# Optimization experiments

Measured on AMD Instinct MI355X. Metric: run time of the kernel, lower is better.

Reference implementation:

```python
import jax, jax.numpy as jnp
import numpy as np

B, L, E = 4, 2048, 1024
H, D = 16, 64  # heads, head_dim; H*D == E


def setup_inputs() -> dict:
    key = jax.random.key(0)
    ks = jax.random.split(key, 6)
    s = 0.02
    return {
        "x": jax.random.normal(ks[0], (B, L, E), dtype=jnp.float32),
        "Wq": jax.random.normal(ks[1], (E, H * D), dtype=jnp.float32) * s,
        "Wk": jax.random.normal(ks[2], (E, H * D), dtype=jnp.float32) * s,
        "Wv": jax.random.normal(ks[3], (E, H * D), dtype=jnp.float32) * s,
        "Wo": jax.random.normal(ks[4], (H * D, E), dtype=jnp.float32) * s,
        "bo": jax.random.normal(ks[5], (E,), dtype=jnp.float32) * s,
    }


def reference(x, Wq, Wk, Wv, Wo, bo):
    b, l, e = x.shape
    q = (x @ Wq).reshape(b, l, H, D)
    k = (x @ Wk).reshape(b, l, H, D)
    v = (x @ Wv).reshape(b, l, H, D)
    # NOTE: original scales by sqrt(embed_size), not sqrt(head_dim)
    energy = jnp.einsum('nqhd,nkhd->nhqk', q, k)
    attn = jax.nn.softmax(energy / jnp.sqrt(jnp.float32(e)), axis=3)
    out = jnp.einsum('nhql,nlhd->nqhd', attn, v).reshape(b, l, H * D)
    return out @ Wo + bo
```

## Files before the change

### kernel.cpp

```cpp
#include <hip/hip_runtime.h>

#define B_ 4
#define L_ 2048
#define E_ 1024
#define H_ 16
#define D_ 64
#define CSCALE 0.045084960222629414f

typedef short s16x8 __attribute__((ext_vector_type(8)));
typedef short s16x4 __attribute__((ext_vector_type(4)));
typedef float f32x4 __attribute__((ext_vector_type(4)));

__device__ __forceinline__ unsigned short f2bf(float f) {
  union { float f; unsigned int u; } v;
  v.f = f;
  unsigned int u = v.u;
  u += 0x7fffu + ((u >> 16) & 1u);
  return (unsigned short)(u >> 16);
}

__device__ __forceinline__ void async16(const void* g, void* l) {
  __builtin_amdgcn_global_load_lds(
      (__attribute__((address_space(1))) void*)(g),
      (__attribute__((address_space(3))) void*)(l), 16, 0, 0);
}

__global__ void k_prep(const float* __restrict__ x,
                       const float* __restrict__ Wq, const float* __restrict__ Wk,
                       const float* __restrict__ Wv, const float* __restrict__ Wo,
                       unsigned short* __restrict__ xb,
                       unsigned short* __restrict__ Wt, unsigned short* __restrict__ WoT) {
  __shared__ float t[32][33];
  int bid = blockIdx.x, tid = threadIdx.x;
  if (bid < 8192) {
    int i = bid * 256 + tid;
    float4 v = ((const float4*)x)[i];
    ushort4 o;
    o.x = f2bf(v.x); o.y = f2bf(v.y); o.z = f2bf(v.z); o.w = f2bf(v.w);
    ((ushort4*)xb)[i] = o;
    return;
  }
  int tt = bid - 8192;
  int wsel = tt >> 10, tile = tt & 1023;
  const float* in = (wsel == 0) ? Wq : (wsel == 1) ? Wk : (wsel == 2) ? Wv : Wo;
  unsigned short* out = (wsel == 0) ? Wt : (wsel == 1) ? Wt + (1u << 20)
                        : (wsel == 2) ? Wt + (2u << 20) : WoT;
  int bx = tile & 31, by = tile >> 5;
  int tx = tid & 31, ty = tid >> 5;
  int xcol = bx * 32 + tx;
  int y0 = by * 32;
#pragma unroll
  for (int i = 0; i < 4; ++i)
    t[ty + i * 8][tx] = in[(size_t)(y0 + ty + i * 8) * 1024 + xcol];
  __syncthreads();
  int xo = by * 32 + tx;
  int yo0 = bx * 32;
#pragma unroll
  for (int i = 0; i < 4; ++i)
    out[(size_t)(yo0 + ty + i * 8) * 1024 + xo] = f2bf(t[tx][ty + i * 8]);
}

__global__ __launch_bounds__(256) void k_gemm_qkvt(
    const unsigned short* __restrict__ xb, const unsigned short* __restrict__ Wt,
    unsigned short* __restrict__ Qb, unsigned short* __restrict__ Kb,
    unsigned short* __restrict__ Vt) {
  __shared__ __align__(16) unsigned short St[3][2][4096];
  const int bid = blockIdx.x;
  const int tid = threadIdx.x;
  const int w = tid >> 6, lane = tid & 63;
  const int quad = lane >> 4, mrow = lane & 15;
  const bool isQK = bid < 1024;
  int m0, n0;
  const unsigned short *PA, *PB;
  if (isQK) {
    m0 = (bid & 63) * 128;
    n0 = (bid >> 6) * 128;
    PA = xb + (size_t)m0 * 1024;
    PB = Wt + (size_t)n0 * 1024;
  } else {
    int g = bid - 1024;
    m0 = (g & 7) * 128;
    n0 = (g >> 3) * 128;
    PA = Wt + (2u << 20) + (size_t)m0 * 1024;
    PB = xb + (size_t)n0 * 1024;
  }
  const int wr = (w >> 1) * 64, wc = (w & 1) * 64;

  auto issue = [&](int kt, int s) {
    int ktw = kt & 31;
#pragma unroll
    for (int r = 0; r < 2; ++r) {
      int c = r * 256 + tid;
      int row = c >> 2, cc = c & 3;
      async16(PA + (size_t)row * 1024 + ktw * 32 + cc * 8, &St[s][0][c * 8]);
      async16(PB + (size_t)row * 1024 + ktw * 32 + cc * 8, &St[s][1][c * 8]);
    }
  };

  const f32x4 fz = {0.f, 0.f, 0.f, 0.f};
  f32x4 acc[4][4];
#pragma unroll
  for (int a = 0; a < 4; ++a)
#pragma unroll
    for (int b = 0; b < 4; ++b) acc[a][b] = fz;

  issue(0, 0);
  issue(1, 1);

  for (int kt = 0; kt < 32; ++kt) {
    asm volatile("s_waitcnt vmcnt(4)" ::: "memory");
    __builtin_amdgcn_s_barrier();
    asm volatile("" ::: "memory");
    issue(kt + 2, (kt + 2) % 3);
    const unsigned short* As = &St[kt % 3][0][0];
    const unsigned short* Bs = &St[kt % 3][1][0];
    s16x8 a[4], b[4];
#pragma unroll
    for (int mt = 0; mt < 4; ++mt)
      a[mt] = *(const s16x8*)&As[(wr + mt * 16 + mrow) * 32 + quad * 8];
#pragma unroll
    for (int nt = 0; nt < 4; ++nt)
      b[nt] = *(const s16x8*)&Bs[(wc + nt * 16 + mrow) * 32 + quad * 8];
#pragma unroll
    for (int mt = 0; mt < 4; ++mt)
#pragma unroll
      for (int nt = 0; nt < 4; ++nt)
        acc[mt][nt] = __builtin_amdgcn_mfma_f32_16x16x32_bf16(a[mt], b[nt], acc[mt][nt], 0, 0, 0);
  }
  if (isQK) {
#pragma unroll
    for (int mt = 0; mt < 4; ++mt)
#pragma unroll
      for (int nt = 0; nt < 4; ++nt)
#pragma unroll
        for (int i = 0; i < 4; ++i) {
          int row = m0 + wr + mt * 16 + quad * 4 + i;
          int col = n0 + wc + nt * 16 + mrow;
          int bb = row >> 11, l = row & 2047;
          if (col < 1024) {
            int h = col >> 6, d = col & 63;
            Qb[(((size_t)(bb * 16 + h)) * 2048 + l) * 64 + d] = f2bf(acc[mt][nt][i]);
          } else {
            int c2 = col - 1024, h = c2 >> 6, d = c2 & 63;
            Kb[(((size_t)(bb * 16 + h)) * 2048 + l) * 64 + d] = f2bf(acc[mt][nt][i] * CSCALE);
          }
        }
  } else {
#pragma unroll
    for (int mt = 0; mt < 4; ++mt)
#pragma unroll
      for (int nt = 0; nt < 4; ++nt)
#pragma unroll
        for (int i = 0; i < 4; ++i) {
          int f = m0 + wr + mt * 16 + quad * 4 + i;
          int tk = n0 + wc + nt * 16 + mrow;
          int bb = tk >> 11, l = tk & 2047;
          Vt[((size_t)(bb * 1024 + f)) * 2048 + l] = f2bf(acc[mt][nt][i]);
        }
  }
}

struct AK { s16x8 k0, k1; };
struct ST { f32x4 s0, s1; };
struct PAT { s16x4 n0, n1; };

__device__ __forceinline__ AK load_ak(const unsigned short* Kt, int mt, int mrow, int quad) {
  int row = mt * 16 + mrow;
  AK r;
  r.k0 = *(const s16x8*)&Kt[row * 64 + (((0 + quad) ^ (row & 7)) << 3)];
  r.k1 = *(const s16x8*)&Kt[row * 64 + (((4 + quad) ^ (row & 7)) << 3)];
  return r;
}

__device__ __forceinline__ ST qkmm(const AK& a, const s16x8 (&qb)[2][2]) {
  const f32x4 fz = {0.f, 0.f, 0.f, 0.f};
  ST t; t.s0 = fz; t.s1 = fz;
  __builtin_amdgcn_s_setprio(1);
  t.s0 = __builtin_amdgcn_mfma_f32_16x16x32_bf16(a.k0, qb[0][0], t.s0, 0, 0, 0);
  t.s1 = __builtin_amdgcn_mfma_f32_16x16x32_bf16(a.k0, qb[1][0], t.s1, 0, 0, 0);
  t.s0 = __builtin_amdgcn_mfma_f32_16x16x32_bf16(a.k1, qb[0][1], t.s0, 0, 0, 0);
  t.s1 = __builtin_amdgcn_mfma_f32_16x16x32_bf16(a.k1, qb[1][1], t.s1, 0, 0, 0);
  __builtin_amdgcn_s_setprio(0);
  return t;
}

__device__ __forceinline__ s16x4 exp_pack(const f32x4 sv, float& lracc) {
  float p0 = __builtin_amdgcn_exp2f(sv[0]);
  float p1 = __builtin_amdgcn_exp2f(sv[1]);
  float p2 = __builtin_amdgcn_exp2f(sv[2]);
  float p3 = __builtin_amdgcn_exp2f(sv[3]);
  lracc += (p0 + p1) + (p2 + p3);
  unsigned int r01, r23;
  asm("v_cvt_pk_bf16_f32 %0, %1, %2" : "=v"(r01) : "v"(p0), "v"(p1));
  asm("v_cvt_pk_bf16_f32 %0, %1, %2" : "=v"(r23) : "v"(p2), "v"(p3));
  union { unsigned int u[2]; s16x4 v4; } uu;
  uu.u[0] = r01; uu.u[1] = r23;
  return uu.v4;
}

__device__ __forceinline__ PAT expp(const ST& t, float (&lr)[2]) {
  PAT r;
  r.n0 = exp_pack(t.s0, lr[0]);
  r.n1 = exp_pack(t.s1, lr[1]);
  return r;
}

__device__ __forceinline__ void pv(const unsigned short* Vs, int lt, const PAT& p,
                                   f32x4 (&o)[2][4], int mrow, int quad) {
  s16x4 vb[4];
  int lbase = lt * 16 + quad * 4;
  int cg = lbase >> 3, off = lbase & 7;
#pragma unroll
  for (int dt = 0; dt < 4; ++dt) {
    int row = dt * 16 + mrow;
    vb[dt] = *(const s16x4*)&Vs[row * 64 + ((cg ^ (row & 7)) << 3) + off];
  }
  __builtin_amdgcn_s_setprio(1);
#pragma unroll
  for (int dt = 0; dt < 4; ++dt) {
    o[0][dt] = __builtin_amdgcn_mfma_f32_16x16x16bf16_1k(p.n0, vb[dt], o[0][dt], 0, 0, 0);
    o[1][dt] = __builtin_amdgcn_mfma_f32_16x16x16bf16_1k(p.n1, vb[dt], o[1][dt], 0, 0, 0);
  }
  __builtin_amdgcn_s_setprio(0);
}

__global__ __launch_bounds__(512) void k_attn(
    const unsigned short* __restrict__ Qb, const unsigned short* __restrict__ Kb,
    const unsigned short* __restrict__ Vt, unsigned short* __restrict__ AO) {
  __shared__ __align__(16) unsigned short KVs[4][8192];
  const int tid = threadIdx.x, w = tid >> 6, lane = tid & 63;
  const int quad = lane >> 4, mrow = lane & 15;
  const int bh = blockIdx.y;
  const int q0 = blockIdx.x * 256;
  const unsigned short* Qh = Qb + (size_t)bh * 2048 * 64;
  const unsigned short* Kh = Kb + (size_t)bh * 2048 * 64;
  const unsigned short* Vh = Vt + (size_t)bh * 64 * 2048;
  unsigned short* KVf = &KVs[0][0];

#pragma unroll
  for (int r = 0; r < 4; ++r) {
    int c = r * 512 + tid;
    int row = c >> 3, cl = c & 7;
    int gc = cl ^ (row & 7);
    async16(Qh + (size_t)(q0 + row) * 64 + gc * 8, &KVf[c * 8]);
  }
  asm volatile("s_waitcnt vmcnt(0)" ::: "memory");
  __builtin_amdgcn_s_barrier();
  asm volatile("" ::: "memory");
  s16x8 qb[2][2];
#pragma unroll
  for (int nt = 0; nt < 2; ++nt)
#pragma unroll
    for (int ks = 0; ks < 2; ++ks) {
      int row = w * 32 + nt * 16 + mrow;
      qb[nt][ks] = *(const s16x8*)&KVf[row * 64 + (((ks * 4 + quad) ^ (row & 7)) << 3)];
    }
  asm volatile("" ::: "memory");
  __builtin_amdgcn_s_barrier();
  asm volatile("" ::: "memory");

  {
    int row = tid >> 3, cl = tid & 7, gc = cl ^ (row & 7);
    async16(Kh + (size_t)row * 64 + gc * 8, &KVs[0][tid * 8]);
    async16(Vh + (size_t)row * 2048 + gc * 8, &KVs[0][4096 + tid * 8]);
    async16(Kh + (size_t)(64 + row) * 64 + gc * 8, &KVs[1][tid * 8]);
    async16(Vh + (size_t)row * 2048 + 64 + gc * 8, &KVs[1][4096 + tid * 8]);
  }

  const f32x4 fz = {0.f, 0.f, 0.f, 0.f};
  f32x4 o[2][4];
  float lr[2];
#pragma unroll
  for (int nt = 0; nt < 2; ++nt) {
    lr[nt] = 0.f;
#pragma unroll
    for (int dt = 0; dt < 4; ++dt) o[nt][dt] = fz;
  }

  for (int j = 0; j < 32; ++j) {
    {
      int jj = (j + 2) & 31;
      unsigned short* nb = &KVs[(j + 2) & 3][0];
      int row = tid >> 3, cl = tid & 7, gc = cl ^ (row & 7);
      async16(Kh + (size_t)(jj * 64 + row) * 64 + gc * 8, &nb[tid * 8]);
      async16(Vh + (size_t)row * 2048 + jj * 64 + gc * 8, &nb[4096 + tid * 8]);
    }
    asm volatile("s_waitcnt vmcnt(4)" ::: "memory");
    __builtin_amdgcn_s_barrier();
    asm volatile("" ::: "memory");
    const unsigned short* Kt = &KVs[j & 3][0];
    const unsigned short* Vs = &KVs[j & 3][4096];

    AK a0 = load_ak(Kt, 0, mrow, quad); ST t0 = qkmm(a0, qb);
    AK a1 = load_ak(Kt, 1, mrow, quad); ST t1 = qkmm(a1, qb);
    PAT p0 = expp(t0, lr);
    AK a2 = load_ak(Kt, 2, mrow, quad); ST t2 = qkmm(a2, qb);
    pv(Vs, 0, p0, o, mrow, quad);
    PAT p1 = expp(t1, lr);
    AK a3 = load_ak(Kt, 3, mrow, quad); ST t3 = qkmm(a3, qb);
    pv(Vs, 1, p1, o, mrow, quad);
    PAT p2 = expp(t2, lr);
    pv(Vs, 2, p2, o, mrow, quad);
    PAT p3 = expp(t3, lr);
    pv(Vs, 3, p3, o, mrow, quad);
  }

#pragma unroll
  for (int nt = 0; nt < 2; ++nt) {
    float v = lr[nt];
    v += __shfl_xor(v, 16);
    v += __shfl_xor(v, 32);
    lr[nt] = v;
  }

  int b_ = bh >> 4, h = bh & 15;
#pragma unroll
  for (int nt = 0; nt < 2; ++nt)
#pragma unroll
    for (int i = 0; i < 4; ++i) {
      float inv = 1.f / __shfl(lr[nt], quad * 4 + i, 64);
      int qrow = q0 + w * 32 + nt * 16 + quad * 4 + i;
#pragma unroll
      for (int dt = 0; dt < 4; ++dt) {
        int d = dt * 16 + mrow;
        AO[((size_t)(b_ * 2048 + qrow)) * 1024 + h * 64 + d] = f2bf(o[nt][dt][i] * inv);
      }
    }
}

__global__ __launch_bounds__(256) void k_gemm_out(
    const unsigned short* __restrict__ Ab, const unsigned short* __restrict__ WoT,
    const float* __restrict__ bo, float* __restrict__ out) {
  __shared__ __align__(16) unsigned short St[3][2][4096];
  const int tid = threadIdx.x;
  const int w = tid >> 6, lane = tid & 63;
  const int quad = lane >> 4, mrow = lane & 15;
  const int m0 = blockIdx.x * 128, n0 = blockIdx.y * 128;
  const int wr = (w >> 1) * 64, wc = (w & 1) * 64;
  const unsigned short* PA = Ab + (size_t)m0 * 1024;
  const unsigned short* PB = WoT + (size_t)n0 * 1024;

  auto issue = [&](int kt, int s) {
    int ktw = kt & 31;
#pragma unroll
    for (int r = 0; r < 2; ++r) {
      int c = r * 256 + tid;
      int row = c >> 2, cc = c & 3;
      async16(PA + (size_t)row * 1024 + ktw * 32 + cc * 8, &St[s][0][c * 8]);
      async16(PB + (size_t)row * 1024 + ktw * 32 + cc * 8, &St[s][1][c * 8]);
    }
  };

  const f32x4 fz = {0.f, 0.f, 0.f, 0.f};
  f32x4 acc[4][4];
#pragma unroll
  for (int a = 0; a < 4; ++a)
#pragma unroll
    for (int b = 0; b < 4; ++b) acc[a][b] = fz;

  issue(0, 0);
  issue(1, 1);

  for (int kt = 0; kt < 32; ++kt) {
    asm volatile("s_waitcnt vmcnt(4)" ::: "memory");
    __builtin_amdgcn_s_barrier();
    asm volatile("" ::: "memory");
    issue(kt + 2, (kt + 2) % 3);
    const unsigned short* As = &St[kt % 3][0][0];
    const unsigned short* Bs = &St[kt % 3][1][0];
    s16x8 a[4], b[4];
#pragma unroll
    for (int mt = 0; mt < 4; ++mt)
      a[mt] = *(const s16x8*)&As[(wr + mt * 16 + mrow) * 32 + quad * 8];
#pragma unroll
    for (int nt = 0; nt < 4; ++nt)
      b[nt] = *(const s16x8*)&Bs[(wc + nt * 16 + mrow) * 32 + quad * 8];
#pragma unroll
    for (int mt = 0; mt < 4; ++mt)
#pragma unroll
      for (int nt = 0; nt < 4; ++nt)
        acc[mt][nt] = __builtin_amdgcn_mfma_f32_16x16x32_bf16(a[mt], b[nt], acc[mt][nt], 0, 0, 0);
  }
#pragma unroll
  for (int mt = 0; mt < 4; ++mt)
#pragma unroll
    for (int nt = 0; nt < 4; ++nt)
#pragma unroll
      for (int i = 0; i < 4; ++i) {
        int row = m0 + wr + mt * 16 + quad * 4 + i;
        int col = n0 + wc + nt * 16 + mrow;
        out[(size_t)row * 1024 + col] = acc[mt][nt][i] + bo[col];
      }
}

extern "C" void kernel_launch(void* const* d_in, const int* in_sizes, int n_in,
                              void* d_out, int out_size, void* d_ws, size_t ws_size,
                              hipStream_t stream) {
  const float* x  = (const float*)d_in[0];
  const float* Wq = (const float*)d_in[1];
  const float* Wk = (const float*)d_in[2];
  const float* Wv = (const float*)d_in[3];
  const float* Wo = (const float*)d_in[4];
  const float* bo = (const float*)d_in[5];
  float* out = (float*)d_out;

  char* ws = (char*)d_ws;
  const size_t MiB = 1u << 20;
  unsigned short* xb  = (unsigned short*)(ws);
  unsigned short* Wt  = (unsigned short*)(ws + 16 * MiB);
  unsigned short* WoT = (unsigned short*)(ws + 22 * MiB);
  unsigned short* Qb  = (unsigned short*)(ws + 24 * MiB);
  unsigned short* Kb  = (unsigned short*)(ws + 40 * MiB);
  unsigned short* Vt  = (unsigned short*)(ws + 56 * MiB);
  unsigned short* AO  = xb;

  k_prep<<<12288, 256, 0, stream>>>(x, Wq, Wk, Wv, Wo, xb, Wt, WoT);
  k_gemm_qkvt<<<1536, 256, 0, stream>>>(xb, Wt, Qb, Kb, Vt);
  k_attn<<<dim3(8, 64), 512, 0, stream>>>(Qb, Kb, Vt, AO);
  k_gemm_out<<<dim3(64, 8), 256, 0, stream>>>(AO, WoT, bo, out);
}
```

Before: 275.0 us.

## Switch attention inner loop to 32x32x16 MFMA with MFMA-computed row sums

```diff
diff --git a/kernel.cpp b/kernel.cpp
--- a/kernel.cpp
+++ b/kernel.cpp
@@ -10,6 +10,8 @@
 typedef short s16x8 __attribute__((ext_vector_type(8)));
 typedef short s16x4 __attribute__((ext_vector_type(4)));
 typedef float f32x4 __attribute__((ext_vector_type(4)));
+typedef float f32x16 __attribute__((ext_vector_type(16)));
+typedef unsigned int u32;
 
 __device__ __forceinline__ unsigned short f2bf(float f) {
   union { float f; unsigned int u; } v;
@@ -160,68 +162,35 @@
   }
 }
 
-struct AK { s16x8 k0, k1; };
-struct ST { f32x4 s0, s1; };
-struct PAT { s16x4 n0, n1; };
-
-__device__ __forceinline__ AK load_ak(const unsigned short* Kt, int mt, int mrow, int quad) {
-  int row = mt * 16 + mrow;
-  AK r;
-  r.k0 = *(const s16x8*)&Kt[row * 64 + (((0 + quad) ^ (row & 7)) << 3)];
-  r.k1 = *(const s16x8*)&Kt[row * 64 + (((4 + quad) ^ (row & 7)) << 3)];
+__device__ __forceinline__ u32 pkbf(float a, float b) {
+  u32 r;
+  asm("v_cvt_pk_bf16_f32 %0, %1, %2" : "=v"(r) : "v"(a), "v"(b));
   return r;
 }
 
-__device__ __forceinline__ ST qkmm(const AK& a, const s16x8 (&qb)[2][2]) {
-  const f32x4 fz = {0.f, 0.f, 0.f, 0.f};
-  ST t; t.s0 = fz; t.s1 = fz;
-  __builtin_amdgcn_s_setprio(1);
-  t.s0 = __builtin_amdgcn_mfma_f32_16x16x32_bf16(a.k0, qb[0][0], t.s0, 0, 0, 0);
-  t.s1 = __builtin_amdgcn_mfma_f32_16x16x32_bf16(a.k0, qb[1][0], t.s1, 0, 0, 0);
-  t.s0 = __builtin_amdgcn_mfma_f32_16x16x32_bf16(a.k1, qb[0][1], t.s0, 0, 0, 0);
-  t.s1 = __builtin_amdgcn_mfma_f32_16x16x32_bf16(a.k1, qb[1][1], t.s1, 0, 0, 0);
-  __builtin_amdgcn_s_setprio(0);
-  return t;
-}
-
-__device__ __forceinline__ s16x4 exp_pack(const f32x4 sv, float& lracc) {
-  float p0 = __builtin_amdgcn_exp2f(sv[0]);
-  float p1 = __builtin_amdgcn_exp2f(sv[1]);
-  float p2 = __builtin_amdgcn_exp2f(sv[2]);
-  float p3 = __builtin_amdgcn_exp2f(sv[3]);
-  lracc += (p0 + p1) + (p2 + p3);
-  unsigned int r01, r23;
-  asm("v_cvt_pk_bf16_f32 %0, %1, %2" : "=v"(r01) : "v"(p0), "v"(p1));
-  asm("v_cvt_pk_bf16_f32 %0, %1, %2" : "=v"(r23) : "v"(p2), "v"(p3));
-  union { unsigned int u[2]; s16x4 v4; } uu;
-  uu.u[0] = r01; uu.u[1] = r23;
-  return uu.v4;
-}
-
-__device__ __forceinline__ PAT expp(const ST& t, float (&lr)[2]) {
-  PAT r;
-  r.n0 = exp_pack(t.s0, lr[0]);
-  r.n1 = exp_pack(t.s1, lr[1]);
-  return r;
-}
-
-__device__ __forceinline__ void pv(const unsigned short* Vs, int lt, const PAT& p,
-                                   f32x4 (&o)[2][4], int mrow, int quad) {
-  s16x4 vb[4];
-  int lbase = lt * 16 + quad * 4;
-  int cg = lbase >> 3, off = lbase & 7;
-#pragma unroll
-  for (int dt = 0; dt < 4; ++dt) {
-    int row = dt * 16 + mrow;
-    vb[dt] = *(const s16x4*)&Vs[row * 64 + ((cg ^ (row & 7)) << 3) + off];
-  }
-  __builtin_amdgcn_s_setprio(1);
-#pragma unroll
-  for (int dt = 0; dt < 4; ++dt) {
-    o[0][dt] = __builtin_amdgcn_mfma_f32_16x16x16bf16_1k(p.n0, vb[dt], o[0][dt], 0, 0, 0);
-    o[1][dt] = __builtin_amdgcn_mfma_f32_16x16x16bf16_1k(p.n1, vb[dt], o[1][dt], 0, 0, 0);
-  }
-  __builtin_amdgcn_s_setprio(0);
+__device__ __forceinline__ void exp_repack(const f32x16 s, int hi,
+                                           s16x8& paLo, s16x8& paHi) {
+  float p[16];
+#pragma unroll
+  for (int r = 0; r < 16; ++r) p[r] = __builtin_amdgcn_exp2f(s[r]);
+  u32 u[8];
+#pragma unroll
+  for (int t = 0; t < 8; ++t) u[t] = pkbf(p[2 * t], p[2 * t + 1]);
+#pragma unroll
+  for (int cc = 0; cc < 2; ++cc) {
+    u32 X0 = hi ? u[cc * 4 + 2] : u[cc * 4 + 0];
+    u32 X1 = hi ? u[cc * 4 + 3] : u[cc * 4 + 1];
+    u32 Y0 = hi ? u[cc * 4 + 0] : u[cc * 4 + 2];
+    u32 Y1 = hi ? u[cc * 4 + 1] : u[cc * 4 + 3];
+    u32 Z0 = (u32)__shfl_xor((int)Y0, 32, 64);
+    u32 Z1 = (u32)__shfl_xor((int)Y1, 32, 64);
+    union { u32 w[4]; s16x8 v; } f;
+    f.w[0] = hi ? Z0 : X0;
+    f.w[1] = hi ? Z1 : X1;
+    f.w[2] = hi ? X0 : Z0;
+    f.w[3] = hi ? X1 : Z1;
+    if (cc == 0) paLo = f.v; else paHi = f.v;
+  }
 }
 
 __global__ __launch_bounds__(512) void k_attn(
@@ -229,7 +198,7 @@
     const unsigned short* __restrict__ Vt, unsigned short* __restrict__ AO) {
   __shared__ __align__(16) unsigned short KVs[4][8192];
   const int tid = threadIdx.x, w = tid >> 6, lane = tid & 63;
-  const int quad = lane >> 4, mrow = lane & 15;
+  const int lo5 = lane & 31, hi = lane >> 5;
   const int bh = blockIdx.y;
   const int q0 = blockIdx.x * 256;
   const unsigned short* Qh = Qb + (size_t)bh * 2048 * 64;
@@ -247,14 +216,13 @@
   asm volatile("s_waitcnt vmcnt(0)" ::: "memory");
   __builtin_amdgcn_s_barrier();
   asm volatile("" ::: "memory");
-  s16x8 qb[2][2];
-#pragma unroll
-  for (int nt = 0; nt < 2; ++nt)
-#pragma unroll
-    for (int ks = 0; ks < 2; ++ks) {
-      int row = w * 32 + nt * 16 + mrow;
-      qb[nt][ks] = *(const s16x8*)&KVf[row * 64 + (((ks * 4 + quad) ^ (row & 7)) << 3)];
-    }
+  s16x8 qb[4];
+  {
+    int row = w * 32 + lo5, sw = row & 7;
+#pragma unroll
+    for (int c = 0; c < 4; ++c)
+      qb[c] = *(const s16x8*)&KVf[row * 64 + (((2 * c + hi) ^ sw) << 3)];
+  }
   asm volatile("" ::: "memory");
   __builtin_amdgcn_s_barrier();
   asm volatile("" ::: "memory");
@@ -267,15 +235,10 @@
     async16(Vh + (size_t)row * 2048 + 64 + gc * 8, &KVs[1][4096 + tid * 8]);
   }
 
-  const f32x4 fz = {0.f, 0.f, 0.f, 0.f};
-  f32x4 o[2][4];
-  float lr[2];
-#pragma unroll
-  for (int nt = 0; nt < 2; ++nt) {
-    lr[nt] = 0.f;
-#pragma unroll
-    for (int dt = 0; dt < 4; ++dt) o[nt][dt] = fz;
-  }
+  f32x16 o0, o1, osum;
+#pragma unroll
+  for (int i = 0; i < 16; ++i) { o0[i] = 0.f; o1[i] = 0.f; osum[i] = 0.f; }
+  const s16x8 ones = {0x3F80, 0x3F80, 0x3F80, 0x3F80, 0x3F80, 0x3F80, 0x3F80, 0x3F80};
 
   for (int j = 0; j < 32; ++j) {
     {
@@ -291,41 +254,52 @@
     const unsigned short* Kt = &KVs[j & 3][0];
     const unsigned short* Vs = &KVs[j & 3][4096];
 
-    AK a0 = load_ak(Kt, 0, mrow, quad); ST t0 = qkmm(a0, qb);
-    AK a1 = load_ak(Kt, 1, mrow, quad); ST t1 = qkmm(a1, qb);
-    PAT p0 = expp(t0, lr);
-    AK a2 = load_ak(Kt, 2, mrow, quad); ST t2 = qkmm(a2, qb);
-    pv(Vs, 0, p0, o, mrow, quad);
-    PAT p1 = expp(t1, lr);
-    AK a3 = load_ak(Kt, 3, mrow, quad); ST t3 = qkmm(a3, qb);
-    pv(Vs, 1, p1, o, mrow, quad);
-    PAT p2 = expp(t2, lr);
-    pv(Vs, 2, p2, o, mrow, quad);
-    PAT p3 = expp(t3, lr);
-    pv(Vs, 3, p3, o, mrow, quad);
-  }
-
-#pragma unroll
-  for (int nt = 0; nt < 2; ++nt) {
-    float v = lr[nt];
-    v += __shfl_xor(v, 16);
-    v += __shfl_xor(v, 32);
-    lr[nt] = v;
+    s16x8 ak0[4], ak1[4], vb0[4], vb1[4];
+    {
+      int r0 = lo5, s0w = r0 & 7, r1 = 32 + lo5, s1w = r1 & 7;
+#pragma unroll
+      for (int c = 0; c < 4; ++c) {
+        ak0[c] = *(const s16x8*)&Kt[r0 * 64 + (((2 * c + hi) ^ s0w) << 3)];
+        ak1[c] = *(const s16x8*)&Kt[r1 * 64 + (((2 * c + hi) ^ s1w) << 3)];
+        vb0[c] = *(const s16x8*)&Vs[r0 * 64 + (((2 * c + hi) ^ s0w) << 3)];
+        vb1[c] = *(const s16x8*)&Vs[r1 * 64 + (((2 * c + hi) ^ s1w) << 3)];
+      }
+    }
+
+    f32x16 s0, s1;
+#pragma unroll
+    for (int i = 0; i < 16; ++i) { s0[i] = 0.f; s1[i] = 0.f; }
+    __builtin_amdgcn_s_setprio(1);
+#pragma unroll
+    for (int c = 0; c < 4; ++c) {
+      s0 = __builtin_amdgcn_mfma_f32_32x32x16_bf16(ak0[c], qb[c], s0, 0, 0, 0);
+      s1 = __builtin_amdgcn_mfma_f32_32x32x16_bf16(ak1[c], qb[c], s1, 0, 0, 0);
+    }
+    __builtin_amdgcn_s_setprio(0);
+
+    s16x8 pa[4];
+    exp_repack(s0, hi, pa[0], pa[1]);
+    exp_repack(s1, hi, pa[2], pa[3]);
+
+    __builtin_amdgcn_s_setprio(1);
+#pragma unroll
+    for (int c = 0; c < 4; ++c) {
+      o0 = __builtin_amdgcn_mfma_f32_32x32x16_bf16(pa[c], vb0[c], o0, 0, 0, 0);
+      o1 = __builtin_amdgcn_mfma_f32_32x32x16_bf16(pa[c], vb1[c], o1, 0, 0, 0);
+      osum = __builtin_amdgcn_mfma_f32_32x32x16_bf16(pa[c], ones, osum, 0, 0, 0);
+    }
+    __builtin_amdgcn_s_setprio(0);
   }
 
   int b_ = bh >> 4, h = bh & 15;
 #pragma unroll
-  for (int nt = 0; nt < 2; ++nt)
-#pragma unroll
-    for (int i = 0; i < 4; ++i) {
-      float inv = 1.f / __shfl(lr[nt], quad * 4 + i, 64);
-      int qrow = q0 + w * 32 + nt * 16 + quad * 4 + i;
-#pragma unroll
-      for (int dt = 0; dt < 4; ++dt) {
-        int d = dt * 16 + mrow;
-        AO[((size_t)(b_ * 2048 + qrow)) * 1024 + h * 64 + d] = f2bf(o[nt][dt][i] * inv);
-      }
-    }
+  for (int i = 0; i < 16; ++i) {
+    float inv = 1.f / osum[i];
+    int qrow = q0 + w * 32 + (i & 3) + 8 * (i >> 2) + 4 * hi;
+    size_t base = ((size_t)(b_ * 2048 + qrow)) * 1024 + h * 64 + lo5;
+    AO[base] = f2bf(o0[i] * inv);
+    AO[base + 32] = f2bf(o1[i] * inv);
+  }
 }
 
 __global__ __launch_bounds__(256) void k_gemm_out(
```

Result: no change. 276.0 us (+0.4%).
